# Kernel tuning notes

Hardware: AMD Instinct MI355X
Metric: run time of the kernel (lower is better)

The kernel has to match this reference:

```python
import jax, jax.numpy as jnp
import numpy as np

B, S, D, H = 4, 1024, 1024, 16
DH = D // H


def _ln(x, g, b, eps=1e-5):
    m = x.mean(-1, keepdims=True)
    v = ((x - m) ** 2).mean(-1, keepdims=True)
    return (x - m) / jnp.sqrt(v + eps) * g + b


def setup_inputs() -> dict:
    key = jax.random.key(0)
    ks = jax.random.split(key, 8)
    s = 0.02
    return {
        "x": jax.random.normal(ks[0], (B, S, D), jnp.float32),
        # attention projections (bias=False). Stored as [in, out] = torch W.T
        "Wq": jax.random.normal(ks[1], (D, D), jnp.float32) * s,
        "Wk": jax.random.normal(ks[2], (D, D), jnp.float32) * s,
        "Wv": jax.random.normal(ks[3], (D, D), jnp.float32) * s,
        # LayerNorms: ln_start, ln_add_left, ln_add_right, ln_ff
        "g0": jnp.ones((D,), jnp.float32), "b0": jnp.zeros((D,), jnp.float32),
        "gl": jnp.ones((D,), jnp.float32), "bl": jnp.zeros((D,), jnp.float32),
        "gr": jnp.ones((D,), jnp.float32), "br": jnp.zeros((D,), jnp.float32),
        "gf": jnp.ones((D,), jnp.float32), "bf": jnp.zeros((D,), jnp.float32),
        # FF: fc1, fc2 are dim_H -> dim_H with bias
        "W1": jax.random.normal(ks[4], (D, D), jnp.float32) * s,
        "b1": jnp.zeros((D,), jnp.float32),
        "W2": jax.random.normal(ks[5], (D, D), jnp.float32) * s,
        "b2": jnp.zeros((D,), jnp.float32),
    }


def _block(x, Wq, Wk, Wv, g0, b0, gl, bl, gr, br, gf, bf, W1, b1, W2, b2):
    b, s, d = x.shape
    # --- ResiDual MHA ---
    x_ln = _ln(x, g0, b0)
    q = (x_ln @ Wq).reshape(b, s, H, DH)
    k = (x_ln @ Wk).reshape(b, s, H, DH)
    v = (x_ln @ Wv).reshape(b, s, H, DH)
    scores = jnp.einsum("bqhd,bkhd->bhqk", q, k) / np.sqrt(DH).astype(np.float32)
    attn = jax.nn.softmax(scores, axis=-1)
    o = jnp.einsum("bhqk,bkhd->bqhd", attn, v).reshape(b, s, d)
    # note: fc_o is defined in the module but never applied in forward
    left = _ln(x_ln + o, gl, bl)   # ln_add_left
    right = _ln(x + o, gr, br)     # ln_add_right (original residual)
    y = left + right
    # --- FF (pre_ln=False -> ln is Identity), erf GELU ---
    h = y @ W1 + b1
    h = h * 0.5 * (1.0 + jax.lax.erf(h / np.sqrt(2.0).astype(np.float32)))
    y = y + (h @ W2 + b2)
    # --- ln_ff ---
    return _ln(y, gf, bf)


def reference(x, Wq, Wk, Wv, g0, b0, gl, bl, gr, br, gf, bf, W1, b1, W2, b2):
    return _block(x, Wq, Wk, Wv, g0, b0, gl, bl, gr, br, gf, bf, W1, b1, W2, b2)
```

## Files before the change

### kernel.cpp

```cpp
#include <hip/hip_runtime.h>
#include <hip/hip_bf16.h>

typedef __attribute__((ext_vector_type(8))) short bf16x8;
typedef __attribute__((ext_vector_type(4))) float f32x4;
typedef __attribute__((ext_vector_type(4))) short s16x4;

#define DEV static __device__ __forceinline__

DEV short f2bf(float f) {
    unsigned u = __builtin_bit_cast(unsigned, f);
    unsigned r = (u + 0x7fffu + ((u >> 16) & 1u)) >> 16;
    return (short)r;
}

DEV float bf2f(short s) {
    return __builtin_bit_cast(float, ((unsigned)(unsigned short)s) << 16);
}

DEV unsigned pk_bf16(float lo, float hi) {
    __hip_bfloat162 h = __float22bfloat162_rn(make_float2(lo, hi));
    unsigned u;
    __builtin_memcpy(&u, &h, 4);
    return u;
}

DEV void gl_lds16(const void* g, void* l) {
    __builtin_amdgcn_global_load_lds(
        (const __attribute__((address_space(1))) unsigned*)g,
        (__attribute__((address_space(3))) unsigned*)l, 16, 0, 0);
}

DEV float wave_sum(float v) {
    #pragma unroll
    for (int off = 32; off; off >>= 1) v += __shfl_down(v, off, 64);
    return v;
}

DEV float block_sum(float v, float* sm, int t) {
    v = wave_sum(v);
    if ((t & 63) == 0) sm[t >> 6] = v;
    __syncthreads();
    float r = sm[0] + sm[1] + sm[2] + sm[3];
    __syncthreads();
    return r;
}

__global__ __launch_bounds__(256) void transpose_all(
    const float* __restrict__ Wq, const float* __restrict__ Wk,
    const float* __restrict__ Wv, const float* __restrict__ W1,
    const float* __restrict__ W2, short* __restrict__ wqkvT,
    short* __restrict__ w1T, short* __restrict__ w2T, float qscale) {
    __shared__ float tile[32][33];
    const int z = blockIdx.z;
    const float* W;
    short* out;
    float scale = 1.f;
    if (z == 0)      { W = Wq; out = wqkvT;           scale = qscale; }
    else if (z == 1) { W = Wk; out = wqkvT + 1048576; }
    else if (z == 2) { W = Wv; out = wqkvT + 2097152; }
    else if (z == 3) { W = W1; out = w1T; }
    else             { W = W2; out = w2T; }
    int t = threadIdx.x;
    int tx = t & 31, ty = t >> 5;
    int bx = blockIdx.x, by = blockIdx.y;
    #pragma unroll
    for (int i = 0; i < 4; i++) {
        int k = by * 32 + ty + i * 8;
        tile[ty + i * 8][tx] = W[(size_t)k * 1024 + bx * 32 + tx];
    }
    __syncthreads();
    #pragma unroll
    for (int i = 0; i < 4; i++) {
        int n = bx * 32 + ty + i * 8;
        int k = by * 32 + tx;
        out[(size_t)n * 1024 + k] = f2bf(tile[tx][ty + i * 8] * scale);
    }
}

__global__ __launch_bounds__(256) void ln0_kernel(const float* __restrict__ x,
                                                  const float* __restrict__ g,
                                                  const float* __restrict__ b,
                                                  short* __restrict__ xbf) {
    __shared__ float sm[4];
    int row = blockIdx.x, t = threadIdx.x;
    const f32x4 v = *(const f32x4*)(x + (size_t)row * 1024 + t * 4);
    float mean = block_sum(v[0] + v[1] + v[2] + v[3], sm, t) * 0.0009765625f;
    f32x4 d;
    float sq = 0.f;
    #pragma unroll
    for (int j = 0; j < 4; j++) { d[j] = v[j] - mean; sq += d[j] * d[j]; }
    float var = block_sum(sq, sm, t) * 0.0009765625f;
    float inv = rsqrtf(var + 1e-5f);
    const f32x4 gv = *(const f32x4*)(g + t * 4);
    const f32x4 bv = *(const f32x4*)(b + t * 4);
    s16x4 ob;
    #pragma unroll
    for (int j = 0; j < 4; j++) ob[j] = f2bf(d[j] * inv * gv[j] + bv[j]);
    *(s16x4*)(xbf + (size_t)row * 1024 + t * 4) = ob;
}

__global__ __launch_bounds__(256) void ln_dual_kernel(
    const float* __restrict__ x, const short* __restrict__ xln,
    const short* __restrict__ o, const float* __restrict__ gl,
    const float* __restrict__ bl, const float* __restrict__ gr,
    const float* __restrict__ br, short* __restrict__ ybf) {
    __shared__ float sm[4];
    int row = blockIdx.x, t = threadIdx.x;
    size_t base = (size_t)row * 1024 + t * 4;
    const f32x4 xv = *(const f32x4*)(x + base);
    const s16x4 xl = *(const s16x4*)(xln + base);
    const s16x4 ob = *(const s16x4*)(o + base);
    f32x4 u, w;
    #pragma unroll
    for (int j = 0; j < 4; j++) {
        float ov = bf2f(ob[j]);
        u[j] = bf2f(xl[j]) + ov; w[j] = xv[j] + ov;
    }
    float mu = block_sum(u[0] + u[1] + u[2] + u[3], sm, t) * 0.0009765625f;
    float mw = block_sum(w[0] + w[1] + w[2] + w[3], sm, t) * 0.0009765625f;
    float squ = 0.f, sqw = 0.f;
    #pragma unroll
    for (int j = 0; j < 4; j++) {
        u[j] -= mu; squ += u[j] * u[j];
        w[j] -= mw; sqw += w[j] * w[j];
    }
    float iu = rsqrtf(block_sum(squ, sm, t) * 0.0009765625f + 1e-5f);
    float iw = rsqrtf(block_sum(sqw, sm, t) * 0.0009765625f + 1e-5f);
    const f32x4 glv = *(const f32x4*)(gl + t * 4);
    const f32x4 blv = *(const f32x4*)(bl + t * 4);
    const f32x4 grv = *(const f32x4*)(gr + t * 4);
    const f32x4 brv = *(const f32x4*)(br + t * 4);
    s16x4 yb;
    #pragma unroll
    for (int j = 0; j < 4; j++)
        yb[j] = f2bf(u[j] * iu * glv[j] + blv[j] + w[j] * iw * grv[j] + brv[j]);
    *(s16x4*)(ybf + base) = yb;
}

__global__ __launch_bounds__(256) void ln_final_kernel(const short* __restrict__ z,
                                                       const float* __restrict__ g,
                                                       const float* __restrict__ b,
                                                       float* __restrict__ out) {
    __shared__ float sm[4];
    int row = blockIdx.x, t = threadIdx.x;
    const s16x4 zv = *(const s16x4*)(z + (size_t)row * 1024 + t * 4);
    f32x4 v;
    #pragma unroll
    for (int j = 0; j < 4; j++) v[j] = bf2f(zv[j]);
    float mean = block_sum(v[0] + v[1] + v[2] + v[3], sm, t) * 0.0009765625f;
    f32x4 d;
    float sq = 0.f;
    #pragma unroll
    for (int j = 0; j < 4; j++) { d[j] = v[j] - mean; sq += d[j] * d[j]; }
    float var = block_sum(sq, sm, t) * 0.0009765625f;
    float inv = rsqrtf(var + 1e-5f);
    const f32x4 gv = *(const f32x4*)(g + t * 4);
    const f32x4 bv = *(const f32x4*)(b + t * 4);
    f32x4 o;
    #pragma unroll
    for (int j = 0; j < 4; j++) o[j] = d[j] * inv * gv[j] + bv[j];
    *(f32x4*)(out + (size_t)row * 1024 + t * 4) = o;
}

template <int MODE, int BN>
__global__ __launch_bounds__(256, 3) void gemm_bt(
    const short* __restrict__ A, const short* __restrict__ Bt,
    short* __restrict__ outq, short* __restrict__ outk, short* __restrict__ outvt,
    const float* __restrict__ bias, short* __restrict__ outbf,
    const short* __restrict__ yresid, short* __restrict__ outz) {
    constexpr int NF = BN / 32;
    __shared__ short As[128 * 64];
    __shared__ short Bs[BN * 64];
    const int t = threadIdx.x;
    const int lane = t & 63;
    const int w = t >> 6;
    const int wr = w >> 1, wc = w & 1;
    const int l16 = lane & 15, lhi = lane >> 4;
    const int m0 = blockIdx.x * 128;
    const int n0 = blockIdx.y * BN;

    f32x4 acc[4][NF] = {};

    for (int kt = 0; kt < 1024; kt += 64) {
        __syncthreads();
        #pragma unroll
        for (int i = 0; i < 4; i++) {
            int tt = i * 256 + t;
            int row = tt >> 3, c = tt & 7;
            int sw = ((c ^ (row & 7)) << 4);
            gl_lds16((const char*)A + ((size_t)(m0 + row) * 1024 + kt) * 2 + sw,
                     (char*)As + i * 4096 + w * 1024);
        }
        #pragma unroll
        for (int i = 0; i < BN / 32; i++) {
            int tt = i * 256 + t;
            int row = tt >> 3, c = tt & 7;
            int sw = ((c ^ (row & 7)) << 4);
            gl_lds16((const char*)Bt + ((size_t)(n0 + row) * 1024 + kt) * 2 + sw,
                     (char*)Bs + i * 4096 + w * 1024);
        }
        __syncthreads();
        #pragma unroll
        for (int ks = 0; ks < 2; ks++) {
            bf16x8 af[4], bfr[NF];
            #pragma unroll
            for (int mi = 0; mi < 4; mi++) {
                int row = wr * 64 + mi * 16 + l16;
                int c = (ks * 4 + lhi) ^ (row & 7);
                af[mi] = *(const bf16x8*)((const char*)As + row * 128 + c * 16);
            }
            #pragma unroll
            for (int ni = 0; ni < NF; ni++) {
                int row = wc * (BN / 2) + ni * 16 + l16;
                int c = (ks * 4 + lhi) ^ (row & 7);
                bfr[ni] = *(const bf16x8*)((const char*)Bs + row * 128 + c * 16);
            }
            #pragma unroll
            for (int mi = 0; mi < 4; mi++)
                #pragma unroll
                for (int ni = 0; ni < NF; ni++)
                    acc[mi][ni] = __builtin_amdgcn_mfma_f32_16x16x32_bf16(
                        af[mi], bfr[ni], acc[mi][ni], 0, 0, 0);
        }
    }

    #pragma unroll
    for (int mi = 0; mi < 4; mi++) {
        #pragma unroll
        for (int ni = 0; ni < NF; ni++) {
            #pragma unroll
            for (int r = 0; r < 4; r++) {
                int m = m0 + wr * 64 + mi * 16 + lhi * 4 + r;
                int n = n0 + wc * (BN / 2) + ni * 16 + l16;
                float vacc = acc[mi][ni][r];
                if (MODE == 0) {
                    int which = n >> 10, nn = n & 1023;
                    int h = nn >> 6, dh = nn & 63;
                    int b = m >> 10, s = m & 1023;
                    int bh = b * 16 + h;
                    if (which == 0)
                        outq[((size_t)bh * 1024 + s) * 64 + dh] = f2bf(vacc);
                    else if (which == 1)
                        outk[((size_t)bh * 1024 + s) * 64 + dh] = f2bf(vacc);
                    else
                        outvt[((size_t)bh * 64 + dh) * 1024 + s] = f2bf(vacc);
                } else if (MODE == 1) {
                    float hv = vacc + bias[n];
                    float ge = hv * 0.5f * (1.f + erff(hv * 0.70710678118654752f));
                    outbf[(size_t)m * 1024 + n] = f2bf(ge);
                } else {
                    float zz = vacc + bias[n] + bf2f(yresid[(size_t)m * 1024 + n]);
                    outz[(size_t)m * 1024 + n] = f2bf(zz);
                }
            }
        }
    }
}

__global__ __launch_bounds__(512, 4) void attn_kernel(
    const short* __restrict__ qb, const short* __restrict__ kb,
    const short* __restrict__ vtb, short* __restrict__ obuf) {
    __shared__ short Ks[2 * 64 * 64];
    __shared__ short Vs[2 * 64 * 64];
    __shared__ short Ps[8 * 16 * 64];

    const int t = threadIdx.x, lane = t & 63, w = t >> 6;
    const int l16 = lane & 15, lhi = lane >> 4;
    const int blk = blockIdx.x;
    const int qt = (blk >> 3) & 7;
    const int bh = (blk & 7) * 8 + (blk >> 6);
    const short* kp = kb + (size_t)bh * 65536;
    const short* vp = vtb + (size_t)bh * 65536;

    const short* qp = qb + (size_t)bh * 65536 + (size_t)(qt * 128 + w * 16 + l16) * 64;
    bf16x8 qfr[2];
    qfr[0] = *(const bf16x8*)(qp + lhi * 8);
    qfr[1] = *(const bf16x8*)(qp + 32 + lhi * 8);

    f32x4 o[4] = {};
    float mrun = -3.0e38f, lrun = 0.f;

    const int srow = t >> 3, sc8 = t & 7;
    const int ssw = ((sc8 ^ (srow & 7)) << 4);

    gl_lds16((const char*)kp + (size_t)srow * 128 + ssw, (char*)Ks + w * 1024);
    gl_lds16((const char*)vp + (size_t)srow * 2048 + ssw, (char*)Vs + w * 1024);

    short* pw = Ps + w * 1024;
    int cur = 0;

    for (int kv = 0; kv < 16; kv++) {
        asm volatile("s_waitcnt vmcnt(0)");
        __syncthreads();
        if (kv < 15) {
            int nb = cur ^ 1;
            gl_lds16((const char*)kp + (size_t)((kv + 1) * 64 + srow) * 128 + ssw,
                     (char*)Ks + nb * 8192 + w * 1024);
            gl_lds16((const char*)vp + (size_t)srow * 2048 + (kv + 1) * 128 + ssw,
                     (char*)Vs + nb * 8192 + w * 1024);
        }
        const char* kbase = (const char*)Ks + cur * 8192;
        const char* vbase = (const char*)Vs + cur * 8192;

        f32x4 sc[4];
        __builtin_amdgcn_s_setprio(1);
        #pragma unroll
        for (int kvb = 0; kvb < 4; kvb++) {
            f32x4 s4 = {};
            #pragma unroll
            for (int c = 0; c < 2; c++) {
                int row = kvb * 16 + l16;
                int cc = (c * 4 + lhi) ^ (row & 7);
                bf16x8 kf = *(const bf16x8*)(kbase + row * 128 + cc * 16);
                s4 = __builtin_amdgcn_mfma_f32_16x16x32_bf16(kf, qfr[c], s4, 0, 0, 0);
            }
            sc[kvb] = s4;
        }
        __builtin_amdgcn_s_setprio(0);

        float mt = fmaxf(fmaxf(fmaxf(sc[0][0], sc[0][1]), fmaxf(sc[0][2], sc[0][3])),
                         fmaxf(fmaxf(sc[1][0], sc[1][1]), fmaxf(sc[1][2], sc[1][3])));
        mt = fmaxf(mt,
                   fmaxf(fmaxf(fmaxf(sc[2][0], sc[2][1]), fmaxf(sc[2][2], sc[2][3])),
                         fmaxf(fmaxf(sc[3][0], sc[3][1]), fmaxf(sc[3][2], sc[3][3]))));
        mt = fmaxf(mt, __shfl_xor(mt, 16, 64));
        mt = fmaxf(mt, __shfl_xor(mt, 32, 64));

        if (!__all(mt <= mrun + 8.0f)) {
            float nm = fmaxf(mrun, mt);
            float corr = __builtin_amdgcn_exp2f(mrun - nm);
            mrun = nm;
            lrun *= corr;
            #pragma unroll
            for (int r = 0; r < 4; r++) {
                float cr = __shfl(corr, lhi * 4 + r, 64);
                #pragma unroll
                for (int d = 0; d < 4; d++) o[d][r] *= cr;
            }
        }

        float rs = 0.f;
        #pragma unroll
        for (int kvb = 0; kvb < 4; kvb++) {
            #pragma unroll
            for (int r = 0; r < 4; r++) {
                float p = __builtin_amdgcn_exp2f(sc[kvb][r] - mrun);
                sc[kvb][r] = p;
                rs += p;
            }
        }
        rs += __shfl_xor(rs, 16, 64);
        rs += __shfl_xor(rs, 32, 64);
        lrun += rs;

        #pragma unroll
        for (int kvb = 0; kvb < 4; kvb++) {
            uint2 pk;
            pk.x = pk_bf16(sc[kvb][0], sc[kvb][1]);
            pk.y = pk_bf16(sc[kvb][2], sc[kvb][3]);
            int bytecol = kvb * 32 + lhi * 8;
            int addr = l16 * 128 + ((((bytecol >> 4) ^ (l16 & 7)) << 4)) + (bytecol & 15);
            *(uint2*)((char*)pw + addr) = pk;
        }

        bf16x8 pa[2];
        #pragma unroll
        for (int c = 0; c < 2; c++) {
            int cc = (c * 4 + lhi) ^ (l16 & 7);
            pa[c] = *(const bf16x8*)((const char*)pw + l16 * 128 + cc * 16);
        }
        __builtin_amdgcn_s_setprio(1);
        #pragma unroll
        for (int d = 0; d < 4; d++) {
            #pragma unroll
            for (int c = 0; c < 2; c++) {
                int vrow = d * 16 + l16;
                int cc = (c * 4 + lhi) ^ (vrow & 7);
                bf16x8 vf = *(const bf16x8*)(vbase + vrow * 128 + cc * 16);
                o[d] = __builtin_amdgcn_mfma_f32_16x16x32_bf16(pa[c], vf, o[d], 0, 0, 0);
            }
        }
        __builtin_amdgcn_s_setprio(0);
        cur ^= 1;
    }

    const int b = bh >> 4, h = bh & 15;
    float linv[4];
    #pragma unroll
    for (int r = 0; r < 4; r++) linv[r] = 1.0f / __shfl(lrun, lhi * 4 + r, 64);
    #pragma unroll
    for (int d = 0; d < 4; d++) {
        #pragma unroll
        for (int r = 0; r < 4; r++) {
            int s = qt * 128 + w * 16 + lhi * 4 + r;
            int dh = d * 16 + l16;
            obuf[((size_t)(b * 1024 + s)) * 1024 + h * 64 + dh] = f2bf(o[d][r] * linv[r]);
        }
    }
}

extern "C" void kernel_launch(void* const* d_in, const int* in_sizes, int n_in,
                              void* d_out, int out_size, void* d_ws, size_t ws_size,
                              hipStream_t stream) {
    const float* x  = (const float*)d_in[0];
    const float* Wq = (const float*)d_in[1];
    const float* Wk = (const float*)d_in[2];
    const float* Wv = (const float*)d_in[3];
    const float* g0 = (const float*)d_in[4];
    const float* b0 = (const float*)d_in[5];
    const float* gl = (const float*)d_in[6];
    const float* bl = (const float*)d_in[7];
    const float* gr = (const float*)d_in[8];
    const float* br = (const float*)d_in[9];
    const float* gf = (const float*)d_in[10];
    const float* bfp = (const float*)d_in[11];
    const float* W1 = (const float*)d_in[12];
    const float* b1 = (const float*)d_in[13];
    const float* W2 = (const float*)d_in[14];
    const float* b2 = (const float*)d_in[15];

    char* ws = (char*)d_ws;
    short* xlnbf = (short*)(ws);
    short* wqkvT = (short*)(ws + ((size_t)8 << 20));
    short* w1T   = (short*)(ws + ((size_t)14 << 20));
    short* w2T   = (short*)(ws + ((size_t)16 << 20));
    short* qb    = (short*)(ws + ((size_t)18 << 20));
    short* kb    = (short*)(ws + ((size_t)26 << 20));
    short* vtb   = (short*)(ws + ((size_t)34 << 20));
    short* obuf  = (short*)(ws + ((size_t)42 << 20));
    short* ybf   = (short*)(ws + ((size_t)50 << 20));
    short* hbf   = (short*)(ws + ((size_t)58 << 20));
    short* zbf   = (short*)(ws + ((size_t)66 << 20));

    dim3 b256(256);
    transpose_all<<<dim3(32, 32, 5), b256, 0, stream>>>(Wq, Wk, Wv, W1, W2,
                                                        wqkvT, w1T, w2T,
                                                        0.180336880f);

    ln0_kernel<<<4096, b256, 0, stream>>>(x, g0, b0, xlnbf);

    gemm_bt<0, 128><<<dim3(32, 24), b256, 0, stream>>>(
        xlnbf, wqkvT, qb, kb, vtb, nullptr, nullptr, nullptr, nullptr);

    attn_kernel<<<512, dim3(512), 0, stream>>>(qb, kb, vtb, obuf);

    ln_dual_kernel<<<4096, b256, 0, stream>>>(x, xlnbf, obuf, gl, bl, gr, br, ybf);

    gemm_bt<1, 64><<<dim3(32, 16), b256, 0, stream>>>(
        ybf, w1T, nullptr, nullptr, nullptr, b1, hbf, nullptr, nullptr);

    gemm_bt<2, 64><<<dim3(32, 16), b256, 0, stream>>>(
        hbf, w2T, nullptr, nullptr, nullptr, b2, nullptr, ybf, zbf);

    ln_final_kernel<<<4096, b256, 0, stream>>>(zbf, gf, bfp, (float*)d_out);
}
```

Before: 137.1 us.

## Stage V-transpose stores through LDS and double KV tile size in attention

In the QKV GEMM, blocks producing V now write the bf16 accumulator tile into shared memory transposed, then emit coalesced 16-byte stores to the V^T buffer instead of scattered 2-byte strided writes. The attention kernel loads 128-row K/V tiles per iteration, halving the number of barrier/wait iterations, and processes each tile in two 64-column sub-steps. This adds LDS usage in attention (larger double buffers), which may reduce occupancy.

After: 131.5 us. 1.04x faster.

```diff
diff --git a/kernel.cpp b/kernel.cpp
--- a/kernel.cpp
+++ b/kernel.cpp
@@ -169,8 +169,9 @@
     const float* __restrict__ bias, short* __restrict__ outbf,
     const short* __restrict__ yresid, short* __restrict__ outz) {
     constexpr int NF = BN / 32;
-    __shared__ short As[128 * 64];
-    __shared__ short Bs[BN * 64];
+    __shared__ short SH[128 * 64 + BN * 64];
+    short* As = SH;
+    short* Bs = SH + 128 * 64;
     const int t = threadIdx.x;
     const int lane = t & 63;
     const int w = t >> 6;
@@ -222,6 +223,38 @@
                     acc[mi][ni] = __builtin_amdgcn_mfma_f32_16x16x32_bf16(
                         af[mi], bfr[ni], acc[mi][ni], 0, 0, 0);
         }
+    }
+
+    if (MODE == 0 && n0 >= 2048) {
+        __syncthreads();
+        #pragma unroll
+        for (int mi = 0; mi < 4; mi++) {
+            #pragma unroll
+            for (int ni = 0; ni < NF; ni++) {
+                int m0l = wr * 64 + mi * 16 + lhi * 4;
+                int n_l = wc * 64 + ni * 16 + l16;
+                s16x4 pk;
+                #pragma unroll
+                for (int r = 0; r < 4; r++) pk[r] = f2bf(acc[mi][ni][r]);
+                int byte = n_l * 256 + ((m0l * 2) ^ ((n_l & 7) << 4));
+                *(s16x4*)((char*)SH + byte) = pk;
+            }
+        }
+        __syncthreads();
+        const int b = m0 >> 10;
+        const int srow0 = m0 & 1023;
+        #pragma unroll
+        for (int it = 0; it < 8; it++) {
+            int n_l = it * 16 + w * 4 + lhi;
+            int chunk = l16;
+            int byte = n_l * 256 + ((chunk * 16) ^ ((n_l & 7) << 4));
+            bf16x8 vv = *(const bf16x8*)((const char*)SH + byte);
+            int nn = n0 - 2048 + n_l;
+            int hh = nn >> 6, dh = nn & 63;
+            int bh = b * 16 + hh;
+            *(bf16x8*)(outvt + ((size_t)bh * 64 + dh) * 1024 + srow0 + chunk * 8) = vv;
+        }
+        return;
     }
 
     #pragma unroll
@@ -240,10 +273,8 @@
                     int bh = b * 16 + h;
                     if (which == 0)
                         outq[((size_t)bh * 1024 + s) * 64 + dh] = f2bf(vacc);
-                    else if (which == 1)
+                    else
                         outk[((size_t)bh * 1024 + s) * 64 + dh] = f2bf(vacc);
-                    else
-                        outvt[((size_t)bh * 64 + dh) * 1024 + s] = f2bf(vacc);
                 } else if (MODE == 1) {
                     float hv = vacc + bias[n];
                     float ge = hv * 0.5f * (1.f + erff(hv * 0.70710678118654752f));
@@ -260,8 +291,8 @@
 __global__ __launch_bounds__(512, 4) void attn_kernel(
     const short* __restrict__ qb, const short* __restrict__ kb,
     const short* __restrict__ vtb, short* __restrict__ obuf) {
-    __shared__ short Ks[2 * 64 * 64];
-    __shared__ short Vs[2 * 64 * 64];
+    __shared__ short Ks[2 * 128 * 64];
+    __shared__ short Vs[2 * 64 * 128];
     __shared__ short Ps[8 * 16 * 64];
 
     const int t = threadIdx.x, lane = t & 63, w = t >> 6;
@@ -280,107 +311,122 @@
     f32x4 o[4] = {};
     float mrun = -3.0e38f, lrun = 0.f;
 
-    const int srow = t >> 3, sc8 = t & 7;
-    const int ssw = ((sc8 ^ (srow & 7)) << 4);
-
-    gl_lds16((const char*)kp + (size_t)srow * 128 + ssw, (char*)Ks + w * 1024);
-    gl_lds16((const char*)vp + (size_t)srow * 2048 + ssw, (char*)Vs + w * 1024);
+    const int krow = t >> 3;
+    const int ksw = (((t & 7) ^ (krow & 7)) << 4);
+    const int vrow = t >> 4;
+    const int vsw = (((t & 15) ^ (vrow & 7)) << 4);
+
+    #pragma unroll
+    for (int i = 0; i < 2; i++) {
+        gl_lds16((const char*)kp + (size_t)(i * 64 + krow) * 128 + ksw,
+                 (char*)Ks + i * 8192 + w * 1024);
+        gl_lds16((const char*)vp + (size_t)(i * 32 + vrow) * 2048 + vsw,
+                 (char*)Vs + i * 8192 + w * 1024);
+    }
 
     short* pw = Ps + w * 1024;
     int cur = 0;
 
-    for (int kv = 0; kv < 16; kv++) {
+    for (int kv = 0; kv < 8; kv++) {
         asm volatile("s_waitcnt vmcnt(0)");
         __syncthreads();
-        if (kv < 15) {
+        if (kv < 7) {
             int nb = cur ^ 1;
-            gl_lds16((const char*)kp + (size_t)((kv + 1) * 64 + srow) * 128 + ssw,
-                     (char*)Ks + nb * 8192 + w * 1024);
-            gl_lds16((const char*)vp + (size_t)srow * 2048 + (kv + 1) * 128 + ssw,
-                     (char*)Vs + nb * 8192 + w * 1024);
-        }
-        const char* kbase = (const char*)Ks + cur * 8192;
-        const char* vbase = (const char*)Vs + cur * 8192;
-
-        f32x4 sc[4];
-        __builtin_amdgcn_s_setprio(1);
-        #pragma unroll
-        for (int kvb = 0; kvb < 4; kvb++) {
-            f32x4 s4 = {};
+            #pragma unroll
+            for (int i = 0; i < 2; i++) {
+                gl_lds16((const char*)kp +
+                             (size_t)((kv + 1) * 128 + i * 64 + krow) * 128 + ksw,
+                         (char*)Ks + nb * 16384 + i * 8192 + w * 1024);
+                gl_lds16((const char*)vp + (size_t)(i * 32 + vrow) * 2048 +
+                             (kv + 1) * 256 + vsw,
+                         (char*)Vs + nb * 16384 + i * 8192 + w * 1024);
+            }
+        }
+        const char* kbase = (const char*)Ks + cur * 16384;
+        const char* vbase = (const char*)Vs + cur * 16384;
+
+        #pragma unroll
+        for (int sub = 0; sub < 2; sub++) {
+            f32x4 sc[4];
+            __builtin_amdgcn_s_setprio(1);
+            #pragma unroll
+            for (int kvb = 0; kvb < 4; kvb++) {
+                f32x4 s4 = {};
+                #pragma unroll
+                for (int c = 0; c < 2; c++) {
+                    int row = sub * 64 + kvb * 16 + l16;
+                    int cc = (c * 4 + lhi) ^ (row & 7);
+                    bf16x8 kf = *(const bf16x8*)(kbase + row * 128 + cc * 16);
+                    s4 = __builtin_amdgcn_mfma_f32_16x16x32_bf16(kf, qfr[c], s4, 0, 0, 0);
+                }
+                sc[kvb] = s4;
+            }
+            __builtin_amdgcn_s_setprio(0);
+
+            float mt = fmaxf(fmaxf(fmaxf(sc[0][0], sc[0][1]), fmaxf(sc[0][2], sc[0][3])),
+                             fmaxf(fmaxf(sc[1][0], sc[1][1]), fmaxf(sc[1][2], sc[1][3])));
+            mt = fmaxf(mt,
+                       fmaxf(fmaxf(fmaxf(sc[2][0], sc[2][1]), fmaxf(sc[2][2], sc[2][3])),
+                             fmaxf(fmaxf(sc[3][0], sc[3][1]), fmaxf(sc[3][2], sc[3][3]))));
+            mt = fmaxf(mt, __shfl_xor(mt, 16, 64));
+            mt = fmaxf(mt, __shfl_xor(mt, 32, 64));
+
+            if (!__all(mt <= mrun + 8.0f)) {
+                float nm = fmaxf(mrun, mt);
+                float corr = __builtin_amdgcn_exp2f(mrun - nm);
+                mrun = nm;
+                lrun *= corr;
+                #pragma unroll
+                for (int r = 0; r < 4; r++) {
+                    float cr = __shfl(corr, lhi * 4 + r, 64);
+                    #pragma unroll
+                    for (int d = 0; d < 4; d++) o[d][r] *= cr;
+                }
+            }
+
+            float rs = 0.f;
+            #pragma unroll
+            for (int kvb = 0; kvb < 4; kvb++) {
+                #pragma unroll
+                for (int r = 0; r < 4; r++) {
+                    float p = __builtin_amdgcn_exp2f(sc[kvb][r] - mrun);
+                    sc[kvb][r] = p;
+                    rs += p;
+                }
+            }
+            rs += __shfl_xor(rs, 16, 64);
+            rs += __shfl_xor(rs, 32, 64);
+            lrun += rs;
+
+            #pragma unroll
+            for (int kvb = 0; kvb < 4; kvb++) {
+                uint2 pk;
+                pk.x = pk_bf16(sc[kvb][0], sc[kvb][1]);
+                pk.y = pk_bf16(sc[kvb][2], sc[kvb][3]);
+                int bytecol = kvb * 32 + lhi * 8;
+                int addr = l16 * 128 + ((((bytecol >> 4) ^ (l16 & 7)) << 4)) + (bytecol & 15);
+                *(uint2*)((char*)pw + addr) = pk;
+            }
+
+            bf16x8 pa[2];
             #pragma unroll
             for (int c = 0; c < 2; c++) {
-                int row = kvb * 16 + l16;
-                int cc = (c * 4 + lhi) ^ (row & 7);
-                bf16x8 kf = *(const bf16x8*)(kbase + row * 128 + cc * 16);
-                s4 = __builtin_amdgcn_mfma_f32_16x16x32_bf16(kf, qfr[c], s4, 0, 0, 0);
-            }
-            sc[kvb] = s4;
-        }
-        __builtin_amdgcn_s_setprio(0);
-
-        float mt = fmaxf(fmaxf(fmaxf(sc[0][0], sc[0][1]), fmaxf(sc[0][2], sc[0][3])),
-                         fmaxf(fmaxf(sc[1][0], sc[1][1]), fmaxf(sc[1][2], sc[1][3])));
-        mt = fmaxf(mt,
-                   fmaxf(fmaxf(fmaxf(sc[2][0], sc[2][1]), fmaxf(sc[2][2], sc[2][3])),
-                         fmaxf(fmaxf(sc[3][0], sc[3][1]), fmaxf(sc[3][2], sc[3][3]))));
-        mt = fmaxf(mt, __shfl_xor(mt, 16, 64));
-        mt = fmaxf(mt, __shfl_xor(mt, 32, 64));
-
-        if (!__all(mt <= mrun + 8.0f)) {
-            float nm = fmaxf(mrun, mt);
-            float corr = __builtin_amdgcn_exp2f(mrun - nm);
-            mrun = nm;
-            lrun *= corr;
-            #pragma unroll
-            for (int r = 0; r < 4; r++) {
-                float cr = __shfl(corr, lhi * 4 + r, 64);
+                int cc = (c * 4 + lhi) ^ (l16 & 7);
+                pa[c] = *(const bf16x8*)((const char*)pw + l16 * 128 + cc * 16);
+            }
+            __builtin_amdgcn_s_setprio(1);
+            #pragma unroll
+            for (int d = 0; d < 4; d++) {
                 #pragma unroll
-                for (int d = 0; d < 4; d++) o[d][r] *= cr;
-            }
-        }
-
-        float rs = 0.f;
-        #pragma unroll
-        for (int kvb = 0; kvb < 4; kvb++) {
-            #pragma unroll
-            for (int r = 0; r < 4; r++) {
-                float p = __builtin_amdgcn_exp2f(sc[kvb][r] - mrun);
-                sc[kvb][r] = p;
-                rs += p;
-            }
-        }
-        rs += __shfl_xor(rs, 16, 64);
-        rs += __shfl_xor(rs, 32, 64);
-        lrun += rs;
-
-        #pragma unroll
-        for (int kvb = 0; kvb < 4; kvb++) {
-            uint2 pk;
-            pk.x = pk_bf16(sc[kvb][0], sc[kvb][1]);
-            pk.y = pk_bf16(sc[kvb][2], sc[kvb][3]);
-            int bytecol = kvb * 32 + lhi * 8;
-            int addr = l16 * 128 + ((((bytecol >> 4) ^ (l16 & 7)) << 4)) + (bytecol & 15);
-            *(uint2*)((char*)pw + addr) = pk;
-        }
-
-        bf16x8 pa[2];
-        #pragma unroll
-        for (int c = 0; c < 2; c++) {
-            int cc = (c * 4 + lhi) ^ (l16 & 7);
-            pa[c] = *(const bf16x8*)((const char*)pw + l16 * 128 + cc * 16);
-        }
-        __builtin_amdgcn_s_setprio(1);
-        #pragma unroll
-        for (int d = 0; d < 4; d++) {
-            #pragma unroll
-            for (int c = 0; c < 2; c++) {
-                int vrow = d * 16 + l16;
-                int cc = (c * 4 + lhi) ^ (vrow & 7);
-                bf16x8 vf = *(const bf16x8*)(vbase + vrow * 128 + cc * 16);
-                o[d] = __builtin_amdgcn_mfma_f32_16x16x32_bf16(pa[c], vf, o[d], 0, 0, 0);
-            }
-        }
-        __builtin_amdgcn_s_setprio(0);
+                for (int c = 0; c < 2; c++) {
+                    int vr = d * 16 + l16;
+                    int sbyte = (sub * 128 + c * 64 + lhi * 16) ^ ((vr & 7) << 4);
+                    bf16x8 vf = *(const bf16x8*)(vbase + vr * 256 + sbyte);
+                    o[d] = __builtin_amdgcn_mfma_f32_16x16x32_bf16(pa[c], vf, o[d], 0, 0, 0);
+                }
+            }
+            __builtin_amdgcn_s_setprio(0);
+        }
         cur ^= 1;
     }
 
```
